# Kernel tuning notes

Measured on AMD Instinct MI355X. Metric: run time of the kernel, lower is better.

## Reference

```python
import jax, jax.numpy as jnp
import numpy as np

GROUP = 5  # in-group size implied by `expected_in = indices.shape[1] * 5`


def setup_inputs() -> dict:
    key = jax.random.key(0)
    k1, k2, k3, k4 = jax.random.split(key, 4)
    T, IN, OUT, G, C, K = 64, 4100, 12288, 820, 2, 256
    x = jax.random.normal(k1, (T, IN), dtype=jnp.float32)
    indices = jax.random.randint(k2, (OUT, G, C), 0, K, dtype=jnp.int32)
    codebooks = (jax.random.normal(k3, (C, K, GROUP), dtype=jnp.float32) * 0.05).astype(jnp.float16)
    scales = jax.random.uniform(k4, (OUT,), dtype=jnp.float32, minval=0.5, maxval=1.5)
    return {"x": x, "indices": indices, "codebooks": codebooks, "scales": scales}


def reference(x, indices, codebooks, scales):
    orig_shape = x.shape
    x_flat = x.reshape(-1, orig_shape[-1])
    expected_in = indices.shape[1] * GROUP
    pad = expected_in - x_flat.shape[1]
    if pad > 0:
        x_flat = jnp.pad(x_flat, ((0, 0), (0, pad)))
    # safety scaling (fp16 overflow guard), as in the torch module
    x_max = jnp.maximum(jnp.abs(x_flat).max(), 1.0) * 8.0
    cb_max = jnp.maximum(jnp.abs(codebooks).astype(jnp.float32).max(), 1.0)
    x_safe = (x_flat / x_max).astype(jnp.float16)
    cb_safe = (codebooks.astype(jnp.float32) / cb_max).astype(jnp.float16)
    # additive-codebook dequant: W[o, g] = sum_c cb_safe[c, indices[o,g,c], :]
    C = cb_safe.shape[0]
    gathered = cb_safe[jnp.arange(C)[None, None, :], indices]  # (O, G, C, GROUP) fp16
    W = gathered.sum(axis=2).reshape(indices.shape[0], -1)     # (O, expected_in) fp16
    out = jnp.einsum('ti,oi->to', x_safe, W, preferred_element_type=jnp.float32)
    out = out * x_max.astype(jnp.float32) * cb_max
    out = out * scales[None, :]
    out = jnp.nan_to_num(out, nan=0.0, posinf=0.0, neginf=0.0)
    return out.reshape(*orig_shape[:-1], -1).astype(x.dtype)
```

## Files before the change

### kernel.cpp

```cpp
#include <hip/hip_runtime.h>
#include <hip/hip_fp16.h>
#include <cstdint>

#define T_DIM 64
#define IN_DIM 4100
#define OUT_DIM 12288
#define G_DIM 820
#define KCODE 256
#define GRP 5
#define KB16 410
#define CHUNKS 41
#define CH_G 20
#define KS_PER_CH 10
#define KSPLIT 4
#define NBLK 192
#define LDS_STRIDE 168

#define XM 64.0f
#define INV_XM 0.015625f

typedef _Float16 f16x8 __attribute__((ext_vector_type(8)));
typedef float f32x4 __attribute__((ext_vector_type(4)));
typedef float f32x16 __attribute__((ext_vector_type(16)));

__device__ __align__(16) _Float16 g_xA[2 * KB16 * 64 * 8];

__device__ __forceinline__ float block_reduce_max(float m, float* sm) {
    for (int off = 32; off > 0; off >>= 1)
        m = fmaxf(m, __shfl_down(m, off));
    int tid = threadIdx.x;
    if ((tid & 63) == 0) sm[tid >> 6] = m;
    __syncthreads();
    float r = fmaxf(fmaxf(sm[0], sm[1]), fmaxf(sm[2], sm[3]));
    __syncthreads();
    return r;
}

__device__ __forceinline__ void barrier_lds_only() {
    __builtin_amdgcn_sched_barrier(0);
    asm volatile("s_waitcnt lgkmcnt(0)" ::: "memory");
    __builtin_amdgcn_sched_barrier(0);
    __builtin_amdgcn_s_barrier();
    __builtin_amdgcn_sched_barrier(0);
}

__global__ void __launch_bounds__(256) k2_quant(const float* __restrict__ x) {
    int gt = blockIdx.x * 256 + threadIdx.x;
    int lane = gt & 63;
    int rest = gt >> 6;
    int kb16 = rest % KB16;
    int t2 = rest / KB16;
    int t = t2 * 32 + (lane & 31);
    int g = kb16 * 2 + (lane >> 5);
    const float* xp = x + (size_t)t * IN_DIM + g * GRP;
    f16x8 v = {};
    #pragma unroll
    for (int j = 0; j < GRP; ++j) v[j] = (_Float16)(xp[j] * INV_XM);
    *(f16x8*)&g_xA[(size_t)gt * 8] = v;
}

__global__ void __launch_bounds__(256, 3) k3_gemm(const void* __restrict__ cbraw,
                                                  const int* __restrict__ indices,
                                                  const float* __restrict__ scales,
                                                  float* __restrict__ out) {
    __shared__ alignas(16) _Float16 w_lds[2][64 * LDS_STRIDE];
    __shared__ f16x8 cb_sh[2 * KCODE];
    __shared__ float sm[4];

    int tid = threadIdx.x;
    int nb = blockIdx.x % NBLK;
    int ksp = blockIdx.x / NBLK;
    int n_base = nb * 64;

    unsigned u0 = *(const unsigned*)cbraw;
    bool is_f32 = (((u0 >> 23) & 0xFF) >= 100);
    float mm = 0.f;
    for (int i = tid; i < 2 * KCODE * GRP; i += 256) {
        float v = is_f32 ? ((const float*)cbraw)[i]
                         : (float)((const _Float16*)cbraw)[i];
        mm = fmaxf(mm, fabsf(v));
    }
    float cbm = fmaxf(block_reduce_max(mm, sm), 1.0f);
    for (int e = tid; e < 2 * KCODE; e += 256) {
        f16x8 v = {};
        #pragma unroll
        for (int j = 0; j < GRP; ++j) {
            float w = is_f32 ? ((const float*)cbraw)[e * GRP + j]
                             : (float)((const _Float16*)cbraw)[e * GRP + j];
            v[j] = (_Float16)(w / cbm);
        }
        cb_sh[e] = v;
    }

    int sro[5], sgl[5];
    #pragma unroll
    for (int j = 0; j < 5; ++j) {
        int s = tid + j * 256;
        sro[j] = s / 20; sgl[j] = s - sro[j] * 20;
    }

    const int c0 = (CHUNKS * ksp) / KSPLIT;
    const int c1 = (CHUNKS * (ksp + 1)) / KSPLIT;
    const int wid = tid >> 6, lane = tid & 63;
    const int wo = wid & 1, wt = wid >> 1;
    const int r32 = lane & 31, h = lane >> 5;

    f32x16 acc = {};
    int2 ic[5], in_[5];
    auto ldidx = [&](int c, int2* d) {
        int g0 = c * CH_G;
        #pragma unroll
        for (int j = 0; j < 5; ++j)
            d[j] = *(const int2*)&indices[(size_t)(n_base + sro[j]) * (G_DIM * 2)
                                          + (size_t)(g0 + sgl[j]) * 2];
    };

    ldidx(c0, ic);
    ldidx(c0 + 1 < c1 ? c0 + 1 : c0, in_);
    __syncthreads();

    for (int c = c0; c < c1; ++c) {
        const int buf = c & 1;
        uint4 ar[KS_PER_CH];
        #pragma unroll
        for (int ks = 0; ks < KS_PER_CH; ++ks)
            ar[ks] = *(const uint4*)
                &g_xA[(size_t)((wt * KB16 + c * KS_PER_CH + ks) * 64 + lane) * 8];

        #pragma unroll
        for (int j = 0; j < 5; ++j) {
            f16x8 w = cb_sh[ic[j].x] + cb_sh[KCODE + ic[j].y];
            *(f16x8*)&w_lds[buf][sro[j] * LDS_STRIDE + sgl[j] * 8] = w;
        }
        #pragma unroll
        for (int j = 0; j < 5; ++j) ic[j] = in_[j];

        barrier_lds_only();

        if (c + 2 < c1) ldidx(c + 2, in_);

        #pragma unroll
        for (int ks = 0; ks < KS_PER_CH; ++ks) {
            f16x8 b = *(const f16x8*)
                &w_lds[buf][(wo * 32 + r32) * LDS_STRIDE + ks * 16 + h * 8];
            acc = __builtin_amdgcn_mfma_f32_32x32x16_f16(*(f16x8*)&ar[ks], b, acc, 0, 0, 0);
        }
    }

    int o = n_base + wo * 32 + r32;
    float sc = scales[o] * (XM * cbm);
    #pragma unroll
    for (int reg = 0; reg < 16; ++reg) {
        int row = (reg & 3) + 8 * (reg >> 2) + 4 * h;
        int t = wt * 32 + row;
        float v = acc[reg] * sc;
        if (!isfinite(v)) v = 0.f;
        atomicAdd(&out[(size_t)t * OUT_DIM + o], v);
    }
}

extern "C" void kernel_launch(void* const* d_in, const int* in_sizes, int n_in,
                              void* d_out, int out_size, void* d_ws, size_t ws_size,
                              hipStream_t stream) {
    const float* x = (const float*)d_in[0];
    const int* indices = (const int*)d_in[1];
    const void* cbraw = (const void*)d_in[2];
    const float* scales = (const float*)d_in[3];
    float* out = (float*)d_out;
    (void)d_ws; (void)ws_size; (void)n_in; (void)in_sizes; (void)out_size;

    k2_quant<<<205, 256, 0, stream>>>(x);
    k3_gemm<<<NBLK * KSPLIT, 256, 0, stream>>>(cbraw, indices, scales, out);
}
```

Before: 142.5 us.

## Stream codebook indices into an LDS ring via direct global-to-LDS loads

Replaces the register-held, two-deep index prefetch with a double-buffered LDS ring filled by global_load_lds, where each wave loads the indices for its own 16 output rows one chunk ahead. A manual vmcnt wait then lets the x-operand loads stay in flight while the current chunk's indices are consumed. This is meant to cut register pressure and index-load latency on the weight-dequant path. It adds LDS usage and lowers the occupancy hint from 3 to 2 blocks per CU. It also relies on a hand-counted vmcnt that must match the number of issued loads.

After: 154.5 us. 8.4% more time.

```diff
diff --git a/kernel.cpp b/kernel.cpp
--- a/kernel.cpp
+++ b/kernel.cpp
@@ -18,6 +18,9 @@
 
 #define XM 64.0f
 #define INV_XM 0.015625f
+
+#define AS1 __attribute__((address_space(1)))
+#define AS3 __attribute__((address_space(3)))
 
 typedef _Float16 f16x8 __attribute__((ext_vector_type(8)));
 typedef float f32x4 __attribute__((ext_vector_type(4)));
@@ -59,12 +62,13 @@
     *(f16x8*)&g_xA[(size_t)gt * 8] = v;
 }
 
-__global__ void __launch_bounds__(256, 3) k3_gemm(const void* __restrict__ cbraw,
+__global__ void __launch_bounds__(256, 2) k3_gemm(const void* __restrict__ cbraw,
                                                   const int* __restrict__ indices,
                                                   const float* __restrict__ scales,
                                                   float* __restrict__ out) {
     __shared__ alignas(16) _Float16 w_lds[2][64 * LDS_STRIDE];
     __shared__ f16x8 cb_sh[2 * KCODE];
+    __shared__ alignas(16) int2 idx_ring[2][4][320];
     __shared__ float sm[4];
 
     int tid = threadIdx.x;
@@ -92,33 +96,42 @@
         cb_sh[e] = v;
     }
 
-    int sro[5], sgl[5];
-    #pragma unroll
-    for (int j = 0; j < 5; ++j) {
-        int s = tid + j * 256;
-        sro[j] = s / 20; sgl[j] = s - sro[j] * 20;
-    }
-
-    const int c0 = (CHUNKS * ksp) / KSPLIT;
-    const int c1 = (CHUNKS * (ksp + 1)) / KSPLIT;
     const int wid = tid >> 6, lane = tid & 63;
     const int wo = wid & 1, wt = wid >> 1;
     const int r32 = lane & 31, h = lane >> 5;
 
-    f32x16 acc = {};
-    int2 ic[5], in_[5];
-    auto ldidx = [&](int c, int2* d) {
-        int g0 = c * CH_G;
+    const int c0 = (CHUNKS * ksp) / KSPLIT;
+    const int c1 = (CHUNKS * (ksp + 1)) / KSPLIT;
+
+    int srow[5], sg[5];
+    #pragma unroll
+    for (int j = 0; j < 5; ++j) {
+        int e = lane + 64 * j;
+        srow[j] = e / 20; sg[j] = e - srow[j] * 20;
+    }
+
+    auto ring_issue = [&](int c) {
+        int cc = (c < c1) ? c : (c1 - 1);
+        int b = c & 1;
+        int g0 = cc * CH_G;
         #pragma unroll
-        for (int j = 0; j < 5; ++j)
-            d[j] = *(const int2*)&indices[(size_t)(n_base + sro[j]) * (G_DIM * 2)
-                                          + (size_t)(g0 + sgl[j]) * 2];
+        for (int j = 0; j < 3; ++j) {
+            int s = j * 64 + lane;
+            if (j < 2 || lane < 32) {
+                int row16 = s / 10, gp = s - row16 * 10;
+                const int2* g = &((const int2*)indices)[
+                    (size_t)(n_base + wid * 16 + row16) * G_DIM + g0 + gp * 2];
+                void* l = (void*)&idx_ring[b][wid][j * 128];
+                __builtin_amdgcn_global_load_lds((const AS1 void*)g, (AS3 void*)l,
+                                                 16, 0, 0);
+            }
+        }
     };
 
-    ldidx(c0, ic);
-    ldidx(c0 + 1 < c1 ? c0 + 1 : c0, in_);
     __syncthreads();
+    ring_issue(c0);
 
+    f32x16 acc = {};
     for (int c = c0; c < c1; ++c) {
         const int buf = c & 1;
         uint4 ar[KS_PER_CH];
@@ -126,19 +139,18 @@
         for (int ks = 0; ks < KS_PER_CH; ++ks)
             ar[ks] = *(const uint4*)
                 &g_xA[(size_t)((wt * KB16 + c * KS_PER_CH + ks) * 64 + lane) * 8];
-
+        __builtin_amdgcn_sched_barrier(0);
+        ring_issue(c + 1);
+        __builtin_amdgcn_sched_barrier(0);
+        asm volatile("s_waitcnt vmcnt(13)" ::: "memory");
+        __builtin_amdgcn_sched_barrier(0);
         #pragma unroll
         for (int j = 0; j < 5; ++j) {
-            f16x8 w = cb_sh[ic[j].x] + cb_sh[KCODE + ic[j].y];
-            *(f16x8*)&w_lds[buf][sro[j] * LDS_STRIDE + sgl[j] * 8] = w;
+            int2 id = idx_ring[buf][wid][srow[j] * 20 + sg[j]];
+            f16x8 wv = cb_sh[id.x] + cb_sh[KCODE + id.y];
+            *(f16x8*)&w_lds[buf][(wid * 16 + srow[j]) * LDS_STRIDE + sg[j] * 8] = wv;
         }
-        #pragma unroll
-        for (int j = 0; j < 5; ++j) ic[j] = in_[j];
-
         barrier_lds_only();
-
-        if (c + 2 < c1) ldidx(c + 2, in_);
-
         #pragma unroll
         for (int ks = 0; ks < KS_PER_CH; ++ks) {
             f16x8 b = *(const f16x8*)
```
